# Kernel optimization log

Measured on AMD Instinct MI355X. Metric: run time of the kernel, lower is better.

## Reference

```python
import jax, jax.numpy as jnp
import numpy as np

B, T, DK, DV, N = 4, 1024, 128, 128, 65536
TOPK = 32

def setup_inputs() -> dict:
    key = jax.random.key(0)
    k1, k2, k3 = jax.random.split(key, 3)
    q = jax.random.normal(k1, (B, T, DK), dtype=jnp.float32)
    keys = jax.random.normal(k2, (N, DK), dtype=jnp.float32)
    values = jax.random.normal(k3, (N, DV), dtype=jnp.float32)
    return {"q": q, "keys": keys, "values": values, "topk": TOPK}

def reference(q, keys, values, topk):
    # scores: [B, T, N] dense dot-product score matrix
    scores = jnp.einsum('btd,nd->btn', q, keys)
    k = min(topk, keys.shape[0])
    _, idx = jax.lax.top_k(scores, k)          # idx: [B, T, k]
    K_mem = keys[idx]                          # [B, T, k, Dk] gather
    V_mem = values[idx]                        # [B, T, k, Dv] gather
    return (K_mem, V_mem)
```

## Files before the change

kernel.cpp:

```cpp
#include <hip/hip_runtime.h>
#include <float.h>

#define NQ      4096
#define NKEYS   65536
#define DKDIM   128
#define DVDIM   128
#define TOPK_N  32
#define NSPLIT  16
#define KPS     (NKEYS / NSPLIT)
#define BQ      64
#define NCAND   (NSPLIT * TOPK_N)
#define NARROW  128
#define NOUT    ((size_t)NQ * TOPK_N * DKDIM)
#define KPT     32
#define NT      (KPS / KPT)

typedef __attribute__((ext_vector_type(8))) short short8;
typedef __attribute__((ext_vector_type(4))) float v4f;

__device__ inline unsigned short f2bf(float f) {
    unsigned int u = __float_as_uint(f);
    return (unsigned short)((u + 0x7FFFu + ((u >> 16) & 1u)) >> 16);
}

__device__ inline unsigned packpk(float s, unsigned li) {
    unsigned u = __float_as_uint(s);
    u = ((int)u < 0) ? ~u : (u | 0x80000000u);
    return (u & 0xFFFFF000u) | (4095u - li);
}
__device__ inline float unpack_lb(unsigned pk) {
    const unsigned m = pk & 0xFFFFF000u;
    const unsigned b = (m & 0x80000000u) ? (m & 0x7FFFFFFFu) : ~m;
    return __uint_as_float(b);
}

#define CEXU(p, s, desc) {                                                  \
    const unsigned _o = (unsigned)__shfl_xor((int)(p), (s));                \
    const bool _first = (p) > _o;                                           \
    const bool _keep  = (_first == (((l16 & (s)) == 0) == (desc)));         \
    (p) = _keep ? (p) : _o; }
#define CEXUI(pa, pb) { if ((pb) > (pa)) { const unsigned _t=(pa); (pa)=(pb); (pb)=_t; } }

__device__ __forceinline__ void sortmergeU(
    unsigned& p0, unsigned& p1, const int cc,
    const unsigned* __restrict__ bqr, const int l16)
{
    unsigned s0 = (l16      < cc) ? bqr[l16]      : 0u;
    unsigned s1 = (l16 + 16 < cc) ? bqr[l16 + 16] : 0u;

    CEXU(s0, 1, ((l16 & 2) == 0)); CEXU(s1, 1, ((l16 & 2) == 0));
    CEXU(s0, 2, ((l16 & 4) == 0)); CEXU(s1, 2, ((l16 & 4) == 0));
    CEXU(s0, 1, ((l16 & 4) == 0)); CEXU(s1, 1, ((l16 & 4) == 0));
    CEXU(s0, 4, ((l16 & 8) == 0)); CEXU(s1, 4, ((l16 & 8) == 0));
    CEXU(s0, 2, ((l16 & 8) == 0)); CEXU(s1, 2, ((l16 & 8) == 0));
    CEXU(s0, 1, ((l16 & 8) == 0)); CEXU(s1, 1, ((l16 & 8) == 0));
    CEXU(s0, 8, true);  CEXU(s1, 8, false);
    CEXU(s0, 4, true);  CEXU(s1, 4, false);
    CEXU(s0, 2, true);  CEXU(s1, 2, false);
    CEXU(s0, 1, true);  CEXU(s1, 1, false);
    CEXUI(s0, s1);
    CEXU(s0, 8, true);  CEXU(s1, 8, true);
    CEXU(s0, 4, true);  CEXU(s1, 4, true);
    CEXU(s0, 2, true);  CEXU(s1, 2, true);
    CEXU(s0, 1, true);  CEXU(s1, 1, true);

    unsigned c0 = (unsigned)__shfl_xor((int)s1, 15);
    unsigned c1 = (unsigned)__shfl_xor((int)s0, 15);

    CEXUI(p0, c0);
    CEXUI(p1, c1);
    CEXUI(p0, p1);
    CEXU(p0, 8, true); CEXU(p1, 8, true);
    CEXU(p0, 4, true); CEXU(p1, 4, true);
    CEXU(p0, 2, true); CEXU(p1, 2, true);
    CEXU(p0, 1, true); CEXU(p1, 1, true);
}

__global__ __launch_bounds__(256) void convert_kernel(
    const float* __restrict__ q, const float* __restrict__ keys,
    unsigned short* __restrict__ qbf, unsigned short* __restrict__ kbf)
{
    const size_t QG = (size_t)NQ * DKDIM / 8;
    const size_t KG = (size_t)NKEYS * DKDIM / 8;
    const size_t g  = (size_t)blockIdx.x * 256 + threadIdx.x;
    if (g >= QG + KG) return;
    const float* src;
    unsigned short* dst;
    if (g < QG) { src = q + g * 8;         dst = qbf + g * 8; }
    else        { const size_t h = g - QG; src = keys + h * 8; dst = kbf + h * 8; }
    const float4 a = ((const float4*)src)[0];
    const float4 b = ((const float4*)src)[1];
    short8 o;
    o[0] = (short)f2bf(a.x); o[1] = (short)f2bf(a.y);
    o[2] = (short)f2bf(a.z); o[3] = (short)f2bf(a.w);
    o[4] = (short)f2bf(b.x); o[5] = (short)f2bf(b.y);
    o[6] = (short)f2bf(b.z); o[7] = (short)f2bf(b.w);
    *(short8*)dst = o;
}

__global__ __launch_bounds__(256, 6) void score_select_kernel(
    const unsigned short* __restrict__ qbf, const unsigned short* __restrict__ kbf,
    unsigned* __restrict__ cand)
{
    __shared__ unsigned short kst[2][KPT * DKDIM];
    __shared__ unsigned bq[BQ][33];

    const int tid  = threadIdx.x;
    const int wave = tid >> 6;
    const int lane = tid & 63;
    const int l16  = lane & 15;
    const int quad = lane >> 4;

    const int lin   = blockIdx.y * gridDim.x + blockIdx.x;
    const int split = ((lin & 7) << 1) | (lin >> 9);
    const int qgrp  = (lin >> 3) & 63;
    const int q0    = qgrp * BQ + wave * 16;
    const int nbase = split * KPS;

    unsigned* __restrict__ bqr = &bq[wave * 16 + l16][0];

    short8 afrag[4];
#pragma unroll
    for (int t = 0; t < 4; ++t)
        afrag[t] = *(const short8*)(qbf + (size_t)(q0 + l16) * DKDIM + t * 32 + quad * 8);

    unsigned pk0[4], pk1[4];
#pragma unroll
    for (int r = 0; r < 4; ++r) { pk0[r] = 0u; pk1[r] = 0u; }
    float vmf = -FLT_MAX;
    int   cnt = 0;

    auto select32 = [&](const v4f a1, const v4f a2, const int n0loc) {
        const int h0 = a1[0] > vmf, h1 = a1[1] > vmf, h2 = a1[2] > vmf, h3 = a1[3] > vmf;
        const int h4 = a2[0] > vmf, h5 = a2[1] > vmf, h6 = a2[2] > vmf, h7 = a2[3] > vmf;
        const int nh = h0 + h1 + h2 + h3 + h4 + h5 + h6 + h7;
        const int s16   = __shfl_xor(nh, 16);
        const int psum  = nh + s16;
        const int sx32  = __shfl_xor(psum, 32);
        const int nhcol = psum + sx32;
        if (__ballot(cnt + nhcol > 32)) {
#pragma unroll
            for (int r = 0; r < 4; ++r) {
                const int cc = __shfl(cnt, quad * 4 + r);
                sortmergeU(pk0[r], pk1[r], cc, &bq[wave * 16 + quad * 4 + r][0], l16);
            }
            const unsigned t0 = (unsigned)__shfl((int)pk1[0], (l16 >> 2) * 16 + 15);
            const unsigned t1 = (unsigned)__shfl((int)pk1[1], (l16 >> 2) * 16 + 15);
            const unsigned t2 = (unsigned)__shfl((int)pk1[2], (l16 >> 2) * 16 + 15);
            const unsigned t3 = (unsigned)__shfl((int)pk1[3], (l16 >> 2) * 16 + 15);
            const unsigned a01 = (l16 & 1) ? t1 : t0;
            const unsigned a23 = (l16 & 1) ? t3 : t2;
            vmf = unpack_lb((l16 & 2) ? a23 : a01);
            cnt = 0;
        }
        int pos = cnt + ((quad & 1) ? s16 : 0) + ((quad & 2) ? sx32 : 0);
        const unsigned lb = (unsigned)(n0loc + quad * 4);
        if (h0) { bqr[pos] = packpk(a1[0], lb);      ++pos; }
        if (h1) { bqr[pos] = packpk(a1[1], lb + 1);  ++pos; }
        if (h2) { bqr[pos] = packpk(a1[2], lb + 2);  ++pos; }
        if (h3) { bqr[pos] = packpk(a1[3], lb + 3);  ++pos; }
        if (h4) { bqr[pos] = packpk(a2[0], lb + 16); ++pos; }
        if (h5) { bqr[pos] = packpk(a2[1], lb + 17); ++pos; }
        if (h6) { bqr[pos] = packpk(a2[2], lb + 18); ++pos; }
        if (h7) { bqr[pos] = packpk(a2[3], lb + 19); }
        cnt += nhcol;
    };

    const unsigned short* ksrc = kbf + (size_t)nbase * DKDIM;
    const int c0 = tid, c1 = tid + 256;
    const int d0 = ((c0 >> 4) * 128) + (((c0 & 15) ^ ((c0 >> 4) & 7)) * 8);
    const int d1 = ((c1 >> 4) * 128) + (((c1 & 15) ^ ((c1 >> 4) & 7)) * 8);

    {
        const short8 a = *(const short8*)(ksrc + c0 * 8);
        const short8 b = *(const short8*)(ksrc + c1 * 8);
        *(short8*)&kst[0][d0] = a;
        *(short8*)&kst[0][d1] = b;
    }
    __syncthreads();

    int cur = 0;
    const int sx = l16 & 7;
    for (int t = 0; t < NT; ++t) {
        short8 nA, nB;
        const bool more = (t + 1 < NT);
        if (more) {
            const unsigned short* s = ksrc + (size_t)(t + 1) * (KPT * DKDIM);
            nA = *(const short8*)(s + c0 * 8);
            nB = *(const short8*)(s + c1 * 8);
        }
        const unsigned short* kr0 = &kst[cur][(l16) * 128];
        const unsigned short* kr1 = &kst[cur][(16 + l16) * 128];
        v4f acc1 = {0.f, 0.f, 0.f, 0.f};
        v4f acc2 = {0.f, 0.f, 0.f, 0.f};
#pragma unroll
        for (int tt = 0; tt < 4; ++tt) {
            const short8 b0 = *(const short8*)(kr0 + ((quad + tt * 4) ^ sx) * 8);
            const short8 b1 = *(const short8*)(kr1 + ((quad + tt * 4) ^ sx) * 8);
            acc1 = __builtin_amdgcn_mfma_f32_16x16x32_bf16(b0, afrag[tt], acc1, 0, 0, 0);
            acc2 = __builtin_amdgcn_mfma_f32_16x16x32_bf16(b1, afrag[tt], acc2, 0, 0, 0);
        }
        select32(acc1, acc2, t * KPT);
        if (more) {
            *(short8*)&kst[cur ^ 1][d0] = nA;
            *(short8*)&kst[cur ^ 1][d1] = nB;
        }
        __syncthreads();
        cur ^= 1;
    }

#pragma unroll
    for (int r = 0; r < 4; ++r) {
        const int cc = __shfl(cnt, quad * 4 + r);
        sortmergeU(pk0[r], pk1[r], cc, &bq[wave * 16 + quad * 4 + r][0], l16);
        const size_t base = ((size_t)(q0 + quad * 4 + r) * NSPLIT + split) * TOPK_N;
        cand[base + l16]      = pk0[r];
        cand[base + 16 + l16] = pk1[r];
    }
}

__global__ __launch_bounds__(512) void rescore_gather_kernel(
    const float* __restrict__ qg, const float* __restrict__ keys,
    const float* __restrict__ values, const unsigned* __restrict__ cand,
    float* __restrict__ out)
{
    __shared__ float    qrow[DKDIM];
    __shared__ unsigned spk[NCAND];
    __shared__ int      spn[NCAND];
    __shared__ float    ssv[NARROW];
    __shared__ int      ssi[NARROW];
    const int bt  = blockIdx.x;
    const int tid = threadIdx.x;

    if (tid < DKDIM) qrow[tid] = qg[(size_t)bt * DKDIM + tid];

    unsigned pk = cand[(size_t)bt * NCAND + tid];
    int      n  = (tid >> 5) * KPS + (int)(4095u - (pk & 0xFFFu));

    for (int k = 2; k <= NCAND; k <<= 1) {
        for (int j = k >> 1; j > 0; j >>= 1) {
            unsigned opk; int on;
            if (j >= 64) {
                __syncthreads();
                spk[tid] = pk; spn[tid] = n;
                __syncthreads();
                opk = spk[tid ^ j]; on = spn[tid ^ j];
            } else {
                opk = (unsigned)__shfl_xor((int)pk, j);
                on  = __shfl_xor(n, j);
            }
            const bool dir  = ((tid & k) == 0);
            const bool mineFirst = (pk > opk) || (pk == opk && n < on);
            const bool keep = (((tid & j) == 0) == (mineFirst == dir));
            if (!keep) { pk = opk; n = on; }
        }
    }
    __syncthreads();

    float sc = -FLT_MAX;
    if (tid < NARROW) {
        const float4* krow = (const float4*)(keys + (size_t)n * DKDIM);
        float s = 0.f;
#pragma unroll
        for (int d4 = 0; d4 < DKDIM / 4; ++d4) {
            const float4 k4 = krow[d4];
            const float4 q4 = *(const float4*)&qrow[4 * d4];
            s = fmaf(q4.x, k4.x, s);
            s = fmaf(q4.y, k4.y, s);
            s = fmaf(q4.z, k4.z, s);
            s = fmaf(q4.w, k4.w, s);
        }
        sc = s;
    } else {
        n = 0x7FFFFFFF;
    }

    for (int k = 2; k <= NARROW; k <<= 1) {
        for (int j = k >> 1; j > 0; j >>= 1) {
            float of; int on;
            if (j >= 64) {
                __syncthreads();
                if (tid < NARROW) { ssv[tid] = sc; ssi[tid] = n; }
                __syncthreads();
                const int p = (tid ^ j) & (NARROW - 1);
                of = ssv[p]; on = ssi[p];
            } else {
                of = __shfl_xor(sc, j);
                on = __shfl_xor(n, j);
            }
            const bool dir  = ((tid & k) == 0);
            const bool mineFirst = (sc > of) || (sc == of && n < on);
            const bool keep = (((tid & j) == 0) == (mineFirst == dir));
            if (!keep) { sc = of; n = on; }
        }
    }

    __syncthreads();
    if (tid < TOPK_N) ssi[tid] = n;
    __syncthreads();

    const int lane = tid & 31;
    const int rb   = tid >> 5;
#pragma unroll
    for (int r = 0; r < 2; ++r) {
        const int row = rb + 16 * r;
        const int nn  = ssi[row];
        const float4 kv = *(const float4*)(keys   + (size_t)nn * DKDIM + 4 * lane);
        const float4 vv = *(const float4*)(values + (size_t)nn * DVDIM + 4 * lane);
        const size_t ob = ((size_t)bt * TOPK_N + row) * DKDIM + 4 * lane;
        *(float4*)(out + ob)        = kv;
        *(float4*)(out + NOUT + ob) = vv;
    }
}

extern "C" void kernel_launch(void* const* d_in, const int* in_sizes, int n_in,
                              void* d_out, int out_size, void* d_ws, size_t ws_size,
                              hipStream_t stream)
{
    const float* q      = (const float*)d_in[0];
    const float* keys   = (const float*)d_in[1];
    const float* values = (const float*)d_in[2];
    float* out = (float*)d_out;

    unsigned short* qbf = (unsigned short*)d_ws;
    unsigned short* kbf = (unsigned short*)((char*)d_ws + (1u << 20));
    unsigned* cand = (unsigned*)((char*)d_ws + (17u << 20));

    const int cvt_groups = (NQ + NKEYS) * DKDIM / 8;
    convert_kernel<<<(cvt_groups + 255) / 256, 256, 0, stream>>>(q, keys, qbf, kbf);
    score_select_kernel<<<dim3(NQ / BQ, NSPLIT), 256, 0, stream>>>(qbf, kbf, cand);
    rescore_gather_kernel<<<NQ, 512, 0, stream>>>(q, keys, values, cand, out);
}
```

Measured before the change: 595.0 us.

## Software-pipeline MFMA scoring with selection and split gather into separate kernel

The score loop now computes the MFMA tile for step t while running top-k selection on the accumulators from step t-1, so matrix-core work can overlap the scalar/branchy select logic. Separately, the rescore kernel now writes only top-k indices, and a new lightweight gather kernel copies key/value rows with one float4 per thread. This adds register pressure for the extra accumulators and one more kernel launch plus an index round-trip through global memory.

```diff
diff --git a/kernel.cpp b/kernel.cpp
--- a/kernel.cpp
+++ b/kernel.cpp
@@ -170,6 +170,22 @@
     const int c0 = tid, c1 = tid + 256;
     const int d0 = ((c0 >> 4) * 128) + (((c0 & 15) ^ ((c0 >> 4) & 7)) * 8);
     const int d1 = ((c1 >> 4) * 128) + (((c1 & 15) ^ ((c1 >> 4) & 7)) * 8);
+    const int sx = l16 & 7;
+
+    auto mfma_tile = [&](int b, v4f& o1, v4f& o2) {
+        const unsigned short* kr0 = &kst[b][(l16) * 128];
+        const unsigned short* kr1 = &kst[b][(16 + l16) * 128];
+        v4f x1 = {0.f, 0.f, 0.f, 0.f};
+        v4f x2 = {0.f, 0.f, 0.f, 0.f};
+#pragma unroll
+        for (int tt = 0; tt < 4; ++tt) {
+            const short8 b0 = *(const short8*)(kr0 + ((quad + tt * 4) ^ sx) * 8);
+            const short8 b1 = *(const short8*)(kr1 + ((quad + tt * 4) ^ sx) * 8);
+            x1 = __builtin_amdgcn_mfma_f32_16x16x32_bf16(b0, afrag[tt], x1, 0, 0, 0);
+            x2 = __builtin_amdgcn_mfma_f32_16x16x32_bf16(b1, afrag[tt], x2, 0, 0, 0);
+        }
+        o1 = x1; o2 = x2;
+    };
 
     {
         const short8 a = *(const short8*)(ksrc + c0 * 8);
@@ -179,9 +195,19 @@
     }
     __syncthreads();
 
-    int cur = 0;
-    const int sx = l16 & 7;
-    for (int t = 0; t < NT; ++t) {
+    v4f accP1, accP2, accC1, accC2;
+    {
+        const unsigned short* s = ksrc + (size_t)(KPT * DKDIM);
+        const short8 nA = *(const short8*)(s + c0 * 8);
+        const short8 nB = *(const short8*)(s + c1 * 8);
+        mfma_tile(0, accP1, accP2);
+        *(short8*)&kst[1][d0] = nA;
+        *(short8*)&kst[1][d1] = nB;
+    }
+    __syncthreads();
+
+    int cur = 1;
+    for (int t = 1; t < NT; ++t) {
         short8 nA, nB;
         const bool more = (t + 1 < NT);
         if (more) {
@@ -189,25 +215,16 @@
             nA = *(const short8*)(s + c0 * 8);
             nB = *(const short8*)(s + c1 * 8);
         }
-        const unsigned short* kr0 = &kst[cur][(l16) * 128];
-        const unsigned short* kr1 = &kst[cur][(16 + l16) * 128];
-        v4f acc1 = {0.f, 0.f, 0.f, 0.f};
-        v4f acc2 = {0.f, 0.f, 0.f, 0.f};
-#pragma unroll
-        for (int tt = 0; tt < 4; ++tt) {
-            const short8 b0 = *(const short8*)(kr0 + ((quad + tt * 4) ^ sx) * 8);
-            const short8 b1 = *(const short8*)(kr1 + ((quad + tt * 4) ^ sx) * 8);
-            acc1 = __builtin_amdgcn_mfma_f32_16x16x32_bf16(b0, afrag[tt], acc1, 0, 0, 0);
-            acc2 = __builtin_amdgcn_mfma_f32_16x16x32_bf16(b1, afrag[tt], acc2, 0, 0, 0);
-        }
-        select32(acc1, acc2, t * KPT);
+        mfma_tile(cur, accC1, accC2);
+        select32(accP1, accP2, (t - 1) * KPT);
         if (more) {
             *(short8*)&kst[cur ^ 1][d0] = nA;
             *(short8*)&kst[cur ^ 1][d1] = nB;
         }
         __syncthreads();
-        cur ^= 1;
-    }
+        accP1 = accC1; accP2 = accC2; cur ^= 1;
+    }
+    select32(accP1, accP2, (NT - 1) * KPT);
 
 #pragma unroll
     for (int r = 0; r < 4; ++r) {
@@ -219,10 +236,9 @@
     }
 }
 
-__global__ __launch_bounds__(512) void rescore_gather_kernel(
+__global__ __launch_bounds__(512) void rescore_kernel(
     const float* __restrict__ qg, const float* __restrict__ keys,
-    const float* __restrict__ values, const unsigned* __restrict__ cand,
-    float* __restrict__ out)
+    const unsigned* __restrict__ cand, int* __restrict__ topi)
 {
     __shared__ float    qrow[DKDIM];
     __shared__ unsigned spk[NCAND];
@@ -295,22 +311,21 @@
         }
     }
 
-    __syncthreads();
-    if (tid < TOPK_N) ssi[tid] = n;
-    __syncthreads();
-
-    const int lane = tid & 31;
-    const int rb   = tid >> 5;
-#pragma unroll
-    for (int r = 0; r < 2; ++r) {
-        const int row = rb + 16 * r;
-        const int nn  = ssi[row];
-        const float4 kv = *(const float4*)(keys   + (size_t)nn * DKDIM + 4 * lane);
-        const float4 vv = *(const float4*)(values + (size_t)nn * DVDIM + 4 * lane);
-        const size_t ob = ((size_t)bt * TOPK_N + row) * DKDIM + 4 * lane;
-        *(float4*)(out + ob)        = kv;
-        *(float4*)(out + NOUT + ob) = vv;
-    }
+    if (tid < TOPK_N) topi[(size_t)bt * TOPK_N + tid] = n;
+}
+
+__global__ __launch_bounds__(256) void gather_kernel(
+    const float* __restrict__ keys, const float* __restrict__ values,
+    const int* __restrict__ topi, float* __restrict__ out)
+{
+    const unsigned g = blockIdx.x * 256 + threadIdx.x;
+    const int lane   = g & 31;
+    const int tensor = (g >> 5) & 1;
+    const unsigned rowid = g >> 6;
+    const int n = topi[rowid];
+    const float* src = (tensor ? values : keys) + (size_t)n * DKDIM + 4 * lane;
+    const size_t ob  = (size_t)tensor * NOUT + (size_t)rowid * DKDIM + 4 * lane;
+    *(float4*)(out + ob) = *(const float4*)src;
 }
 
 extern "C" void kernel_launch(void* const* d_in, const int* in_sizes, int n_in,
@@ -325,9 +340,11 @@
     unsigned short* qbf = (unsigned short*)d_ws;
     unsigned short* kbf = (unsigned short*)((char*)d_ws + (1u << 20));
     unsigned* cand = (unsigned*)((char*)d_ws + (17u << 20));
+    int* topi = (int*)((char*)d_ws + (25u << 20));
 
     const int cvt_groups = (NQ + NKEYS) * DKDIM / 8;
     convert_kernel<<<(cvt_groups + 255) / 256, 256, 0, stream>>>(q, keys, qbf, kbf);
     score_select_kernel<<<dim3(NQ / BQ, NSPLIT), 256, 0, stream>>>(qbf, kbf, cand);
-    rescore_gather_kernel<<<NQ, 512, 0, stream>>>(q, keys, values, cand, out);
-}
+    rescore_kernel<<<NQ, 512, 0, stream>>>(q, keys, cand, topi);
+    gather_kernel<<<(NQ * TOPK_N * 2 * 32) / 256, 256, 0, stream>>>(keys, values, topi, out);
+}
```

Measured after the change: 654.9 us. 10.1% more time.
